# Kernel optimization log

Measured on AMD Instinct MI355X. Metric: run time of the kernel, lower is better.

## Reference

```python
import jax, jax.numpy as jnp
import numpy as np

DENSITY = 0.1  # fraction of nonzero weights kept by the mask


def setup_inputs() -> dict:
    key = jax.random.key(0)
    k_data, k_w, k_m, k_b = jax.random.split(key, 4)
    M, N, K = 8192, 4096, 4096  # tokens, out_features, in_features
    data = jax.random.normal(k_data, (M, K), dtype=jnp.float32)
    weight = jax.random.normal(k_w, (N, K), dtype=jnp.float32)
    mask = (jax.random.uniform(k_m, (N, K)) < DENSITY).astype(jnp.float32)
    bias = jax.random.normal(k_b, (N,), dtype=jnp.float32)
    return {"data": data, "weight": weight, "mask": mask, "bias": bias}


def reference(data, weight, mask, bias):
    # Equivalent to cuSPARSE CSR SpMM with W_sparse = mask * weight, plus bias:
    # out = data @ (mask * weight)^T + bias  (same math as ref_forward / F.linear)
    w = mask * weight  # [N, K]
    out = jnp.einsum('mk,nk->mn', data, w) + bias  # [M, N]
    return out
```

## Files before the change

kernel.cpp:

```cpp
#include <hip/hip_runtime.h>
#include <hip/hip_bf16.h>


#define Mdim 8192
#define Ndim 4096
#define Kdim 4096

typedef __bf16 bf16x8 __attribute__((ext_vector_type(8)));
typedef float f32x4 __attribute__((ext_vector_type(4)));

__device__ inline unsigned short f2bf(float f) {
    union { float f; unsigned u; } v;
    v.f = f;
    unsigned r = v.u + 0x7fffu + ((v.u >> 16) & 1u);
    return (unsigned short)(r >> 16);
}

__device__ inline unsigned pack2(float a, float b) {
    return (unsigned)f2bf(a) | ((unsigned)f2bf(b) << 16);
}

#define GLOAD_LDS16(gp, lp)                                                     \
    __builtin_amdgcn_global_load_lds((const __attribute__((address_space(1))) void*)(gp), \
                                     (__attribute__((address_space(3))) void*)(lp), 16, 0, 0)

__global__ __launch_bounds__(256) void k_cvt_all(const float4* __restrict__ data,
                                                 const float4* __restrict__ weight,
                                                 const float4* __restrict__ mask,
                                                 uint4* __restrict__ Abf,
                                                 uint4* __restrict__ Bbf) {
    const int NA = Mdim * (Kdim / 8);
    const int NB = Ndim * (Kdim / 8);
    const int stride = gridDim.x * blockDim.x;
    for (int i = blockIdx.x * blockDim.x + threadIdx.x; i < NA + NB; i += stride) {
        if (i < NA) {
            const size_t j2 = 2 * (size_t)i;
            float4 v0 = data[j2], v1 = data[j2 + 1];
            uint4 o;
            o.x = pack2(v0.x, v0.y); o.y = pack2(v0.z, v0.w);
            o.z = pack2(v1.x, v1.y); o.w = pack2(v1.z, v1.w);
            Abf[i] = o;
        } else {
            const size_t j = (size_t)(i - NA);
            const size_t j2 = 2 * j;
            float4 w0 = weight[j2], w1 = weight[j2 + 1];
            float4 m0 = mask[j2],   m1 = mask[j2 + 1];
            uint4 o;
            o.x = pack2(w0.x * m0.x, w0.y * m0.y);
            o.y = pack2(w0.z * m0.z, w0.w * m0.w);
            o.z = pack2(w1.x * m1.x, w1.y * m1.y);
            o.w = pack2(w1.z * m1.z, w1.w * m1.w);
            Bbf[j] = o;
        }
    }
}

__global__ __launch_bounds__(256) void k_gemm(const unsigned short* __restrict__ A,
                                              const unsigned short* __restrict__ B,
                                              const float* __restrict__ bias,
                                              float* __restrict__ out) {
    __shared__ unsigned short As[128 * 32];
    __shared__ unsigned short Bs[128 * 32];

    const int tid  = threadIdx.x;
    const int lane = tid & 63;
    const int wave = tid >> 6;
    const int wm   = (wave >> 1) * 64;
    const int wn   = (wave & 1) * 64;
    const int bm   = blockIdx.y * 128;
    const int bn   = blockIdx.x * 128;

    const int ar = lane >> 2;
    const int ac = (lane & 3) * 8;
    const unsigned short* Ag0 = A + (size_t)(bm + wave * 32 + ar) * Kdim + ac;
    const unsigned short* Ag1 = Ag0 + (size_t)16 * Kdim;
    const unsigned short* Bg0 = B + (size_t)(bn + wave * 32 + ar) * Kdim + ac;
    const unsigned short* Bg1 = Bg0 + (size_t)16 * Kdim;
    unsigned short* Al0 = As + wave * 1024 + lane * 8;
    unsigned short* Al1 = Al0 + 512;
    unsigned short* Bl0 = Bs + wave * 1024 + lane * 8;
    unsigned short* Bl1 = Bl0 + 512;

    f32x4 zero = {0.f, 0.f, 0.f, 0.f};
    f32x4 acc[4][4];
#pragma unroll
    for (int i = 0; i < 4; ++i)
#pragma unroll
        for (int j = 0; j < 4; ++j) acc[i][j] = zero;

    const int fr = lane & 15;
    const int fk = (lane >> 4) * 8;

    for (int k0 = 0; k0 < Kdim; k0 += 32) {
        GLOAD_LDS16(Ag0 + k0, Al0);
        GLOAD_LDS16(Ag1 + k0, Al1);
        GLOAD_LDS16(Bg0 + k0, Bl0);
        GLOAD_LDS16(Bg1 + k0, Bl1);
        __syncthreads();

        bf16x8 af[4], bfr[4];
#pragma unroll
        for (int i = 0; i < 4; ++i)
            af[i] = *(const bf16x8*)&As[(wm + i * 16 + fr) * 32 + fk];
#pragma unroll
        for (int j = 0; j < 4; ++j)
            bfr[j] = *(const bf16x8*)&Bs[(wn + j * 16 + fr) * 32 + fk];

#pragma unroll
        for (int i = 0; i < 4; ++i)
#pragma unroll
            for (int j = 0; j < 4; ++j)
                acc[i][j] = __builtin_amdgcn_mfma_f32_16x16x32_bf16(af[i], bfr[j], acc[i][j], 0, 0, 0);

        __syncthreads();
    }

    const int col_base = bn + wn + (lane & 15);
    const int row_base = bm + wm + (lane >> 4) * 4;
#pragma unroll
    for (int j = 0; j < 4; ++j) {
        const int col = col_base + j * 16;
        const float bv = bias[col];
#pragma unroll
        for (int i = 0; i < 4; ++i) {
            const int row = row_base + i * 16;
            float* op = out + (size_t)row * Ndim + col;
#pragma unroll
            for (int r = 0; r < 4; ++r) op[(size_t)r * Ndim] = acc[i][j][r] + bv;
        }
    }
}

__global__ void k_naive(const float* __restrict__ A, const float* __restrict__ W,
                        const float* __restrict__ Msk, const float* __restrict__ bias,
                        float* __restrict__ out) {
    int n = blockIdx.x * blockDim.x + threadIdx.x;
    int m = blockIdx.y;
    if (n >= Ndim) return;
    const float* a = A + (size_t)m * Kdim;
    const float* w = W + (size_t)n * Kdim;
    const float* mk = Msk + (size_t)n * Kdim;
    float s = 0.f;
    for (int k = 0; k < Kdim; ++k) s += a[k] * w[k] * mk[k];
    out[(size_t)m * Ndim + n] = s + bias[n];
}

extern "C" void kernel_launch(void* const* d_in, const int* in_sizes, int n_in,
                              void* d_out, int out_size, void* d_ws, size_t ws_size,
                              hipStream_t stream) {
    const float* data   = (const float*)d_in[0];
    const float* weight = (const float*)d_in[1];
    const float* mask   = (const float*)d_in[2];
    const float* bias   = (const float*)d_in[3];
    float* out = (float*)d_out;

    const size_t needA = (size_t)Mdim * Kdim * 2;
    const size_t needB = (size_t)Ndim * Kdim * 2;
    if (ws_size < needA + needB) {
        dim3 g((Ndim + 255) / 256, Mdim);
        k_naive<<<g, 256, 0, stream>>>(data, weight, mask, bias, out);
        return;
    }

    unsigned short* Abf = (unsigned short*)d_ws;
    unsigned short* Bbf = Abf + (size_t)Mdim * Kdim;

    k_cvt_all<<<4096, 256, 0, stream>>>((const float4*)data, (const float4*)weight,
                                        (const float4*)mask, (uint4*)Abf, (uint4*)Bbf);

    dim3 grid(Ndim / 128, Mdim / 128);
    k_gemm<<<grid, 256, 0, stream>>>(Abf, Bbf, bias, out);
}
```

Measured before the change: 621.3 us.

## Rewrite GEMM as 256x256 tile with multi-buffered LDS pipeline and swizzle

```diff
diff --git a/kernel.cpp b/kernel.cpp
--- a/kernel.cpp
+++ b/kernel.cpp
@@ -23,6 +23,11 @@
 #define GLOAD_LDS16(gp, lp)                                                     \
     __builtin_amdgcn_global_load_lds((const __attribute__((address_space(1))) void*)(gp), \
                                      (__attribute__((address_space(3))) void*)(lp), 16, 0, 0)
+
+#define VMCNT_I(n)  asm volatile("s_waitcnt vmcnt(" #n ")" ::: "memory")
+#define VMCNT(n)    VMCNT_I(n)
+#define FENCE()     asm volatile("" ::: "memory")
+#define BARRIER()   do { FENCE(); __builtin_amdgcn_s_barrier(); FENCE(); } while (0)
 
 __global__ __launch_bounds__(256) void k_cvt_all(const float4* __restrict__ data,
                                                  const float4* __restrict__ weight,
@@ -55,80 +60,161 @@
     }
 }
 
-__global__ __launch_bounds__(256) void k_gemm(const unsigned short* __restrict__ A,
-                                              const unsigned short* __restrict__ B,
-                                              const float* __restrict__ bias,
-                                              float* __restrict__ out) {
-    __shared__ unsigned short As[128 * 32];
-    __shared__ unsigned short Bs[128 * 32];
+__global__ __launch_bounds__(512, 2) void k_gemm256(const unsigned short* __restrict__ A,
+                                                    const unsigned short* __restrict__ B,
+                                                    const float* __restrict__ bias,
+                                                    float* __restrict__ out) {
+    __shared__ __align__(16) unsigned short sh[4 * 16384];
 
     const int tid  = threadIdx.x;
     const int lane = tid & 63;
     const int wave = tid >> 6;
-    const int wm   = (wave >> 1) * 64;
-    const int wn   = (wave & 1) * 64;
-    const int bm   = blockIdx.y * 128;
-    const int bn   = blockIdx.x * 128;
-
-    const int ar = lane >> 2;
-    const int ac = (lane & 3) * 8;
-    const unsigned short* Ag0 = A + (size_t)(bm + wave * 32 + ar) * Kdim + ac;
-    const unsigned short* Ag1 = Ag0 + (size_t)16 * Kdim;
-    const unsigned short* Bg0 = B + (size_t)(bn + wave * 32 + ar) * Kdim + ac;
-    const unsigned short* Bg1 = Bg0 + (size_t)16 * Kdim;
-    unsigned short* Al0 = As + wave * 1024 + lane * 8;
-    unsigned short* Al1 = Al0 + 512;
-    unsigned short* Bl0 = Bs + wave * 1024 + lane * 8;
-    unsigned short* Bl1 = Bl0 + 512;
-
-    f32x4 zero = {0.f, 0.f, 0.f, 0.f};
-    f32x4 acc[4][4];
-#pragma unroll
-    for (int i = 0; i < 4; ++i)
-#pragma unroll
-        for (int j = 0; j < 4; ++j) acc[i][j] = zero;
+
+    const int bid = blockIdx.x;
+    const int swz = (bid & 7) * 64 + (bid >> 3);
+    const int bm  = (swz & 31) * 256;
+    const int bn  = (swz >> 5) * 256;
+
+    const int rrow = lane >> 3;
+    const int scol = ((lane & 7) ^ rrow) * 8;
+    const int ldsl = lane * 8;
+    const int w8   = wave * 8;
+    const int rbB  = (wave >> 2) * 64 + (wave & 3) * 8;
+
+    const int dstA0 = w8 * 64 + ldsl;
+    const int dstA1 = (64 + w8) * 64 + ldsl;
+    const int dstB0 = 8192 + w8 * 64 + ldsl;
+    const int dstB1 = 8192 + (64 + w8) * 64 + ldsl;
 
     const int fr = lane & 15;
-    const int fk = (lane >> 4) * 8;
-
-    for (int k0 = 0; k0 < Kdim; k0 += 32) {
-        GLOAD_LDS16(Ag0 + k0, Al0);
-        GLOAD_LDS16(Ag1 + k0, Al1);
-        GLOAD_LDS16(Bg0 + k0, Bl0);
-        GLOAD_LDS16(Bg1 + k0, Bl1);
-        __syncthreads();
-
-        bf16x8 af[4], bfr[4];
-#pragma unroll
-        for (int i = 0; i < 4; ++i)
-            af[i] = *(const bf16x8*)&As[(wm + i * 16 + fr) * 32 + fk];
-#pragma unroll
-        for (int j = 0; j < 4; ++j)
-            bfr[j] = *(const bf16x8*)&Bs[(wn + j * 16 + fr) * 32 + fk];
-
-#pragma unroll
-        for (int i = 0; i < 4; ++i)
-#pragma unroll
-            for (int j = 0; j < 4; ++j)
-                acc[i][j] = __builtin_amdgcn_mfma_f32_16x16x32_bf16(af[i], bfr[j], acc[i][j], 0, 0, 0);
-
-        __syncthreads();
-    }
-
-    const int col_base = bn + wn + (lane & 15);
-    const int row_base = bm + wm + (lane >> 4) * 4;
-#pragma unroll
-    for (int j = 0; j < 4; ++j) {
-        const int col = col_base + j * 16;
+    const int kc = lane >> 4;
+    const int po = (kc ^ (fr & 7)) * 8;
+    const int arow = ((wave >> 2) * 64 + fr) * 64;
+    const int brow = ((wave & 3) * 32 + fr) * 64;
+
+    const unsigned short* pA0 = A + (size_t)(bm + w8 + rrow) * Kdim + scol;
+    const unsigned short* pA1 = pA0 + (size_t)128 * Kdim;
+    const unsigned short* pA2 = pA0 + (size_t)64 * Kdim;
+    const unsigned short* pA3 = pA0 + (size_t)192 * Kdim;
+    const unsigned short* pB0 = B + (size_t)(bn + rbB + rrow) * Kdim + scol;
+    const unsigned short* pB1 = pB0 + (size_t)128 * Kdim;
+    const unsigned short* pB2 = pB0 + (size_t)32 * Kdim;
+    const unsigned short* pB3 = pB0 + (size_t)160 * Kdim;
+
+    f32x4 acc[8][4];
+#pragma unroll
+    for (int i = 0; i < 8; ++i)
+#pragma unroll
+        for (int j = 0; j < 4; ++j) acc[i][j] = (f32x4){0.f, 0.f, 0.f, 0.f};
+
+    bf16x8 a0[4][2], a1[4][2], b0[2][2], b1[2][2];
+
+#define READ_A4(dst, base) do {                                                  \
+    _Pragma("unroll")                                                            \
+    for (int _i = 0; _i < 4; ++_i) {                                             \
+        dst[_i][0] = *(const bf16x8*)&sh[(base) + _i * 1024 + po];               \
+        dst[_i][1] = *(const bf16x8*)&sh[(base) + _i * 1024 + (po ^ 32)];        \
+    } } while (0)
+
+#define READ_B2(dst, base) do {                                                  \
+    _Pragma("unroll")                                                            \
+    for (int _j = 0; _j < 2; ++_j) {                                             \
+        dst[_j][0] = *(const bf16x8*)&sh[(base) + _j * 1024 + po];               \
+        dst[_j][1] = *(const bf16x8*)&sh[(base) + _j * 1024 + (po ^ 32)];        \
+    } } while (0)
+
+#define Q_MFMA(AF, BF, IO, JO) do {                                              \
+    __builtin_amdgcn_s_setprio(1);                                               \
+    _Pragma("unroll")                                                            \
+    for (int _i = 0; _i < 4; ++_i) {                                             \
+        _Pragma("unroll")                                                        \
+        for (int _j = 0; _j < 2; ++_j) {                                         \
+            acc[(IO)+_i][(JO)+_j] = __builtin_amdgcn_mfma_f32_16x16x32_bf16(     \
+                AF[_i][0], BF[_j][0], acc[(IO)+_i][(JO)+_j], 0, 0, 0);           \
+            acc[(IO)+_i][(JO)+_j] = __builtin_amdgcn_mfma_f32_16x16x32_bf16(     \
+                AF[_i][1], BF[_j][1], acc[(IO)+_i][(JO)+_j], 0, 0, 0);           \
+        } }                                                                      \
+    __builtin_amdgcn_s_setprio(0); } while (0)
+
+#define KTILE(W0_, W1_, W2_, DOSTAGE, DOTAIL, EB, OB, EB2) do {                  \
+                                                     \
+    VMCNT(W0_); BARRIER();                                                       \
+    Q_MFMA(a0, b0, 0, 0);                                                        \
+                                                     \
+    READ_A4(a1, (OB) + arow);                                                    \
+    VMCNT(W1_); BARRIER();                                                       \
+    if (DOSTAGE) {                                                               \
+        GLOAD_LDS16(pA0, sh + (EB) + dstA0);                                     \
+        GLOAD_LDS16(pA1, sh + (EB) + dstA1);                                     \
+        GLOAD_LDS16(pB0, sh + (EB) + dstB0);                                     \
+        GLOAD_LDS16(pB1, sh + (EB) + dstB1);                                     \
+    }                                                                            \
+    Q_MFMA(a1, b0, 4, 0);                                                        \
+                                                     \
+    READ_B2(b1, (OB) + 8192 + brow);                                             \
+    VMCNT(W2_); BARRIER();                                                       \
+    if (DOSTAGE) {                                                               \
+        GLOAD_LDS16(pA2, sh + (OB) + dstA0);                                     \
+        GLOAD_LDS16(pA3, sh + (OB) + dstA1);                                     \
+    }                                                                            \
+    Q_MFMA(a1, b1, 4, 2);                                                        \
+                                                     \
+    BARRIER();                                                                   \
+    if (DOSTAGE) {                                                               \
+        GLOAD_LDS16(pB2, sh + (OB) + dstB0);                                     \
+        GLOAD_LDS16(pB3, sh + (OB) + dstB1);                                     \
+        pA0 += 64; pA1 += 64; pA2 += 64; pA3 += 64;                              \
+        pB0 += 64; pB1 += 64; pB2 += 64; pB3 += 64;                              \
+    }                                                                            \
+    Q_MFMA(a0, b1, 0, 2);                                                        \
+    if (DOTAIL) {        \
+        READ_A4(a0, (EB2) + arow);                                               \
+        READ_B2(b0, (EB2) + 8192 + brow);                                        \
+    } } while (0)
+
+    GLOAD_LDS16(pA0, sh + 0 + dstA0);      GLOAD_LDS16(pA1, sh + 0 + dstA1);
+    GLOAD_LDS16(pB0, sh + 0 + dstB0);      GLOAD_LDS16(pB1, sh + 0 + dstB1);
+    GLOAD_LDS16(pA2, sh + 16384 + dstA0);  GLOAD_LDS16(pA3, sh + 16384 + dstA1);
+    GLOAD_LDS16(pB2, sh + 16384 + dstB0);  GLOAD_LDS16(pB3, sh + 16384 + dstB1);
+    GLOAD_LDS16(pA0 + 64, sh + 32768 + dstA0); GLOAD_LDS16(pA1 + 64, sh + 32768 + dstA1);
+    GLOAD_LDS16(pB0 + 64, sh + 32768 + dstB0); GLOAD_LDS16(pB1 + 64, sh + 32768 + dstB1);
+    GLOAD_LDS16(pA2 + 64, sh + 49152 + dstA0); GLOAD_LDS16(pA3 + 64, sh + 49152 + dstA1);
+    GLOAD_LDS16(pB2 + 64, sh + 49152 + dstB0); GLOAD_LDS16(pB3 + 64, sh + 49152 + dstB1);
+    pA0 += 128; pA1 += 128; pA2 += 128; pA3 += 128;
+    pB0 += 128; pB1 += 128; pB2 += 128; pB3 += 128;
+
+    VMCNT(12);
+    BARRIER();
+    READ_A4(a0, 0 + arow);
+    READ_B2(b0, 0 + 8192 + brow);
+
+    for (int t2 = 0; t2 < 31; ++t2) {
+        KTILE(10, 8, 8, true, true, 0,     16384, 32768);
+        KTILE(10, 8, 8, true, true, 32768, 49152, 0);
+    }
+    KTILE(10, 8, 4, false, true, 0, 16384, 32768);
+    KTILE(2, 0, 0, false, false, 32768, 49152, 0);
+
+    const int wm = (wave >> 2) * 128;
+    const int wn = (wave & 3) * 64;
+    const int colb = bn + wn + fr;
+    const int rowb = bm + wm + (lane >> 4) * 4;
+#pragma unroll
+    for (int jg = 0; jg < 4; ++jg) {
+        const int col = colb + jg * 16;
         const float bv = bias[col];
 #pragma unroll
-        for (int i = 0; i < 4; ++i) {
-            const int row = row_base + i * 16;
+        for (int ig = 0; ig < 8; ++ig) {
+            const int row = rowb + ig * 16;
             float* op = out + (size_t)row * Ndim + col;
 #pragma unroll
-            for (int r = 0; r < 4; ++r) op[(size_t)r * Ndim] = acc[i][j][r] + bv;
+            for (int r = 0; r < 4; ++r) op[(size_t)r * Ndim] = acc[ig][jg][r] + bv;
         }
     }
+#undef KTILE
+#undef Q_MFMA
+#undef READ_A4
+#undef READ_B2
 }
 
 __global__ void k_naive(const float* __restrict__ A, const float* __restrict__ W,
@@ -168,6 +254,5 @@
     k_cvt_all<<<4096, 256, 0, stream>>>((const float4*)data, (const float4*)weight,
                                         (const float4*)mask, (uint4*)Abf, (uint4*)Bbf);
 
-    dim3 grid(Ndim / 128, Mdim / 128);
-    k_gemm<<<grid, 256, 0, stream>>>(Abf, Bbf, bias, out);
-}
+    k_gemm256<<<dim3(512), dim3(512), 0, stream>>>(Abf, Bbf, bias, out);
+}
```

After: 591.7 us. 1.05x faster.
